# Kernel tuning notes

Hardware: AMD Instinct MI355X
Metric: run time of the kernel (lower is better)

## Reference

```python
import jax, jax.numpy as jnp
import numpy as np

N_ATOMS = 32768
N_GRAPHS = 256
PER_GRAPH = 128
HIDDEN = 128
FILTERS = 128
NUM_GAUSS = 50
CUTOFF = 5.0
NUM_LAYERS = 3
OUT_CH = 1
BOX = 14.1
SLOPE = 0.015


def _lrelu(x):
    return jnp.where(x > 0, x, SLOPE * x)


def setup_inputs() -> dict:
    rng = np.random.default_rng(0)
    batch = np.repeat(np.arange(N_GRAPHS), PER_GRAPH).astype(np.int64)
    pos_np = rng.uniform(0.0, BOX, size=(N_ATOMS, 3)).astype(np.float32)
    # radius graph, built per-graph exactly like compute_radius_graph
    # (with global index offset so edges reference global node ids)
    edges = []
    for b in range(N_GRAPHS):
        pb = pos_np[b * PER_GRAPH:(b + 1) * PER_GRAPH]
        d = np.linalg.norm(pb[:, None, :] - pb[None, :, :], axis=-1)
        src, dst = np.where((d <= CUTOFF) & (d > 0))
        edges.append(np.stack([src, dst], axis=0) + b * PER_GRAPH)
    edge_index = np.concatenate(edges, axis=1).astype(np.int64)
    z = rng.integers(0, 100, size=(N_ATOMS,)).astype(np.int64)

    key = jax.random.key(0)
    ks = jax.random.split(key, 12)

    def xavier(k, shape):
        fan_in, fan_out = shape[-2], shape[-1]
        s = float(np.sqrt(6.0 / (fan_in + fan_out)))
        return jax.random.uniform(k, shape, jnp.float32, -s, s)

    L = NUM_LAYERS
    params = dict(
        emb=jax.random.normal(ks[0], (100, HIDDEN), jnp.float32),
        w_lin=xavier(ks[1], (L, HIDDEN, FILTERS)),
        mlp_w1=xavier(ks[2], (L, NUM_GAUSS, FILTERS)), mlp_b1=jnp.zeros((L, FILTERS), jnp.float32),
        mlp_w2=xavier(ks[3], (L, FILTERS, FILTERS)), mlp_b2=jnp.zeros((L, FILTERS), jnp.float32),
        mlp_w3=xavier(ks[4], (L, FILTERS, FILTERS)), mlp_b3=jnp.zeros((L, FILTERS), jnp.float32),
        lout_w=xavier(ks[5], (L, FILTERS, FILTERS)), lout_b=jnp.zeros((L, FILTERS), jnp.float32),
        v_w1=xavier(ks[6], (L, FILTERS, HIDDEN)), v_b1=jnp.zeros((L, HIDDEN), jnp.float32),
        v_w2=xavier(ks[7], (L, HIDDEN, HIDDEN)), v_b2=jnp.zeros((L, HIDDEN), jnp.float32),
        u_w1=xavier(ks[8], (HIDDEN, HIDDEN // 2)), u_b1=jnp.zeros((HIDDEN // 2,), jnp.float32),
        u_w2=xavier(ks[9], (HIDDEN // 2, OUT_CH)), u_b2=jnp.zeros((OUT_CH,), jnp.float32),
    )
    return dict(z=jnp.asarray(z), pos=jnp.asarray(pos_np), batch=jnp.asarray(batch),
                edge_index=jnp.asarray(edge_index), **params)


def reference(z, pos, batch, edge_index, emb, w_lin,
              mlp_w1, mlp_b1, mlp_w2, mlp_b2, mlp_w3, mlp_b3,
              lout_w, lout_b, v_w1, v_b1, v_w2, v_b2,
              u_w1, u_b1, u_w2, u_b2):
    row, col = edge_index[0], edge_index[1]          # row = j (source), col = i (target)
    dist = jnp.linalg.norm(pos[row] - pos[col], axis=-1)        # [E]
    offset = jnp.linspace(0.0, CUTOFF, NUM_GAUSS)
    coeff = -0.5 / (offset[1] - offset[0]) ** 2
    dist_emb = jnp.exp(coeff * (dist[:, None] - offset[None, :]) ** 2)   # [E, G]
    C = 0.5 * (jnp.cos(dist * jnp.pi / CUTOFF) + 1.0)                    # [E]

    v = emb[z]                                                           # [N, H]
    for l in range(NUM_LAYERS):
        # UpdateE: filter MLP on distance embedding, cosine cutoff envelope
        h = _lrelu(dist_emb @ mlp_w1[l] + mlp_b1[l])
        h = _lrelu(h @ mlp_w2[l] + mlp_b2[l])
        W = (h @ mlp_w3[l] + mlp_b3[l]) * C[:, None]                     # [E, F]
        e = (v @ w_lin[l])[row] * W                                      # gather + modulate
        e = (e @ lout_w[l] + lout_b[l]) + e                              # residual edge lin
        # UpdateV: scatter-add into target nodes, then 2-layer MLP residual
        agg = jax.ops.segment_sum(e, col, num_segments=N_ATOMS)         # [N, F]
        v = v + (_lrelu(agg @ v_w1[l] + v_b1[l]) @ v_w2[l] + v_b2[l])

    # UpdateU: node MLP then per-graph mean pooling
    u = _lrelu(v @ u_w1 + u_b1) @ u_w2 + u_b2                            # [N, out]
    sums = jax.ops.segment_sum(u, batch, num_segments=N_GRAPHS)
    cnt = jax.ops.segment_sum(jnp.ones((u.shape[0],), u.dtype), batch, num_segments=N_GRAPHS)
    return jnp.where(cnt[:, None] > 0, sums / jnp.maximum(cnt, 1.0)[:, None], 0.0)
```

## Files before the change

### kernel.cpp

```cpp
#include <hip/hip_runtime.h>

typedef float f4 __attribute__((ext_vector_type(4)));
typedef float f2 __attribute__((ext_vector_type(2)));
typedef float f32x4 __attribute__((ext_vector_type(4)));
typedef short bf16x8 __attribute__((ext_vector_type(8)));
typedef short sh4 __attribute__((ext_vector_type(4)));
typedef unsigned short us4 __attribute__((ext_vector_type(4)));

#define G_TAB 8192
#define SWZ(row, b) ((b) ^ (((row) & 7) << 4))

__device__ __forceinline__ float lrelu(float x) { return x > 0.f ? x : 0.015f * x; }

__device__ __forceinline__ short f2bf(float x) {
  union { float f; unsigned u; } v; v.f = x;
  unsigned r = v.u + 0x7fff + ((v.u >> 16) & 1);
  return (short)(r >> 16);
}
__device__ __forceinline__ float bf2f(short h) {
  union { float f; unsigned u; } v; v.u = ((unsigned)(unsigned short)h) << 16;
  return v.f;
}
__device__ __forceinline__ float bf2fu(unsigned short h) {
  union { float f; unsigned u; } v; v.u = ((unsigned)h) << 16;
  return v.f;
}

__device__ __forceinline__ void st_pair(short* Hi, short* Lo, int row, int k, f4 x) {
  sh4 hi, lo;
  #pragma unroll
  for (int c = 0; c < 4; c++) { hi[c] = f2bf(x[c]); lo[c] = f2bf(x[c] - bf2f(hi[c])); }
  int b = row * 256 + SWZ(row, (k >> 3) * 16) + (k & 7) * 2;
  *(sh4*)((char*)Hi + b) = hi;
  *(sh4*)((char*)Lo + b) = lo;
}
__device__ __forceinline__ void st_pair1(short* Hi, short* Lo, int row, int k, float x) {
  short hi = f2bf(x), lo = f2bf(x - bf2f(hi));
  int b = row * 256 + SWZ(row, (k >> 3) * 16) + (k & 7) * 2;
  *(short*)((char*)Hi + b) = hi;
  *(short*)((char*)Lo + b) = lo;
}

template<int NFC, int CH>
__device__ __forceinline__ void mm16(const short* Ahi, const short* Alo,
    const short* __restrict__ BhT, const short* __restrict__ BlT,
    int w, int l, f32x4* acc) {
  int lr = l & 15, lk = l >> 4;
  #pragma unroll
  for (int fc = 0; fc < NFC; fc++) acc[fc] = (f32x4)0.f;
  #pragma unroll
  for (int ch = 0; ch < CH; ch++) {
    int arow = w * 16 + lr;
    int ab = arow * 256 + SWZ(arow, ch * 64 + lk * 16);
    bf16x8 ah = *(const bf16x8*)((const char*)Ahi + ab);
    bf16x8 al = *(const bf16x8*)((const char*)Alo + ab);
    #pragma unroll
    for (int fc = 0; fc < NFC; fc++) {
      int bcol = fc * 16 + lr;
      int bb = bcol * 256 + SWZ(bcol, ch * 64 + lk * 16);
      bf16x8 bh = *(const bf16x8*)((const char*)BhT + bb);
      bf16x8 bl = *(const bf16x8*)((const char*)BlT + bb);
      acc[fc] = __builtin_amdgcn_mfma_f32_16x16x32_bf16(ah, bh, acc[fc], 0, 0, 0);
      acc[fc] = __builtin_amdgcn_mfma_f32_16x16x32_bf16(al, bh, acc[fc], 0, 0, 0);
      acc[fc] = __builtin_amdgcn_mfma_f32_16x16x32_bf16(ah, bl, acc[fc], 0, 0, 0);
    }
  }
}


__global__ __launch_bounds__(256) void gather_emb(const int* __restrict__ z,
    const float* __restrict__ emb, float* __restrict__ v, int nf4) {
  int i = blockIdx.x * 256 + threadIdx.x;
  if (i >= nf4) return;
  int a = i >> 5, s = i & 31;
  ((f4*)v)[i] = ((const f4*)emb)[z[a] * 32 + s];
}

__global__ __launch_bounds__(256) void edge_geom(const int* __restrict__ ei,
    const float* __restrict__ pos, float* __restrict__ edc, int E) {
  int e = blockIdx.x * 256 + threadIdx.x;
  if (e >= E) return;
  int r = ei[e], c = ei[E + e];
  float dx = pos[3*r] - pos[3*c];
  float dy = pos[3*r+1] - pos[3*c+1];
  float dz = pos[3*r+2] - pos[3*c+2];
  float d = sqrtf(dx*dx + dy*dy + dz*dz);
  edc[2*e] = d;
  edc[2*e+1] = 0.5f * (cosf(d * 0.6283185307179586f) + 1.0f);
}

__global__ __launch_bounds__(256) void make_starts(const int* __restrict__ row,
    int* __restrict__ starts, int E, int N) {
  int i = blockIdx.x * 256 + threadIdx.x;
  if (i > N) return;
  int lo = 0, hi = E;
  while (lo < hi) { int mid = (lo + hi) >> 1; if (row[mid] < i) lo = mid + 1; else hi = mid; }
  starts[i] = lo;
}

__global__ __launch_bounds__(256) void convert_wt(const float* __restrict__ w_lin,
    const float* __restrict__ vw2, const float* __restrict__ uw1,
    const float* __restrict__ mw1, const float* __restrict__ mw2,
    const float* __restrict__ mw3, const float* __restrict__ vw1,
    short* __restrict__ dhi, short* __restrict__ dlo) {
  int y = blockIdx.y;
  int i = blockIdx.x * 256 + threadIdx.x;
  int k = i >> 7, j = i & 127;
  int slot; float x;
  if (y < 3)       { slot = y;     x = w_lin[(size_t)y*16384 + k*128 + j]; }
  else if (y < 6)  { slot = 3 + y; x = vw2[(size_t)(y-3)*16384 + k*128 + j]; }
  else if (y == 6) { slot = 9;     x = (j < 64) ? uw1[k*64 + j] : 0.f; }
  else if (y < 10) { slot = 3 + y; x = mw2[(size_t)(y-7)*16384 + k*128 + j]; }
  else if (y < 13) { slot = 3 + y; x = mw3[(size_t)(y-10)*16384 + k*128 + j]; }
  else if (y < 16) { slot = 3 + y; x = (k < 50) ? mw1[(size_t)(y-13)*6400 + k*128 + j] : 0.f; }
  else             { slot = 3 + y; x = vw1[(size_t)(y-16)*16384 + k*128 + j]; }
  short hi = f2bf(x);
  int ob = j * 256 + (((k >> 3) * 16) ^ ((j & 7) << 4)) + (k & 7) * 2;
  char* bh = (char*)dhi + (size_t)slot * 32768;
  char* bl = (char*)dlo + (size_t)slot * 32768;
  *(short*)(bh + ob) = hi;
  *(short*)(bl + ob) = f2bf(x - bf2f(hi));
}

__global__ __launch_bounds__(128) void make_c1(const float* __restrict__ lball,
    const float* __restrict__ w1all, float* __restrict__ c1all) {
  int l = blockIdx.y;
  const float* lb = lball + (size_t)l * 128;
  const float* w1 = w1all + (size_t)l * 16384;
  int j = threadIdx.x;
  float s = 0.f;
  for (int k = 0; k < 128; k++) s += lb[k] * w1[k * 128 + j];
  c1all[l * 128 + j] = s;
}

__global__ __launch_bounds__(512) void prep_M(const float* __restrict__ loutw,
    short* __restrict__ whiT, short* __restrict__ wloT) {
  __shared__ __align__(16) short Ahi[16384];
  __shared__ __align__(16) short Alo[16384];
  int tid = threadIdx.x;
  int lay = blockIdx.x;
  int w = tid >> 6, l = tid & 63;
  int lr = l & 15, lk = l >> 4;
  int arow = w * 16 + (l >> 2), sub = l & 3;
  const f4* src = (const f4*)(loutw + (size_t)lay*16384 + (size_t)arow*128 + sub*32);
  #pragma unroll
  for (int q = 0; q < 8; q++) {
    f4 x = src[q];
    int kb = sub * 32 + q * 4;
    #pragma unroll
    for (int cc = 0; cc < 4; cc++) if (arow == kb + cc) x[cc] += 1.0f;
    st_pair(Ahi, Alo, arow, kb, x);
  }
  __syncthreads();
  f32x4 acc[8];
  mm16<8,4>(Ahi, Alo, whiT + (size_t)(19+lay)*16384, wloT + (size_t)(19+lay)*16384, w, l, acc);
  char* bh = (char*)whiT + (size_t)(3+lay) * 32768;
  char* bl = (char*)wloT + (size_t)(3+lay) * 32768;
  #pragma unroll
  for (int r = 0; r < 4; r++)
    #pragma unroll
    for (int fc = 0; fc < 8; fc++) {
      int row = w*16 + lk*4 + r, col = fc*16 + lr;
      float val = acc[fc][r];
      short hi = f2bf(val);
      int ob = col * 256 + (((row >> 3) * 16) ^ ((col & 7) << 4)) + (row & 7) * 2;
      *(short*)(bh + ob) = hi;
      *(short*)(bl + ob) = f2bf(val - bf2f(hi));
    }
}

__global__ __launch_bounds__(512) void table_mfma(
    const short* __restrict__ whiT, const short* __restrict__ wloT,
    const float* __restrict__ mb1, const float* __restrict__ mb2,
    const float* __restrict__ mb3, unsigned short* __restrict__ tables) {
  __shared__ __align__(16) short Ahi[16384];
  __shared__ __align__(16) short Alo[16384];
  __shared__ __align__(16) short Bhi[16384];
  __shared__ __align__(16) short Blo[16384];
  int tid = threadIdx.x;
  int lay = blockIdx.y;
  int p0 = blockIdx.x * 128;
  int w = tid >> 6, l = tid & 63;
  int lr = l & 15, lk = l >> 4;
  int prow = w * 16 + (l >> 2), sub = l & 3;
  const float delta = 5.0f / (G_TAB - 1);
  {
    float d = (p0 + prow) * delta;
    #pragma unroll
    for (int q = 0; q < 4; q++) {
      f4 x;
      #pragma unroll
      for (int cc = 0; cc < 4; cc++) {
        int k = sub * 16 + q * 4 + cc;
        float t = d - k * (5.0f / 49.0f);
        x[cc] = (k < 50) ? expf(-48.02f * t * t) : 0.f;
      }
      st_pair(Ahi, Alo, prow, sub * 16 + q * 4, x);
    }
  }
  __syncthreads();
  f32x4 acc[8];
  mm16<8,2>(Ahi, Alo, whiT + (size_t)(16+lay)*16384, wloT + (size_t)(16+lay)*16384, w, l, acc);
  #pragma unroll
  for (int r = 0; r < 4; r++)
    #pragma unroll
    for (int fc = 0; fc < 8; fc++)
      st_pair1(Bhi, Blo, w*16 + lk*4 + r, fc*16 + lr,
               lrelu(acc[fc][r] + mb1[lay*128 + fc*16 + lr]));
  __syncthreads();
  mm16<8,4>(Bhi, Blo, whiT + (size_t)(10+lay)*16384, wloT + (size_t)(10+lay)*16384, w, l, acc);
  #pragma unroll
  for (int r = 0; r < 4; r++)
    #pragma unroll
    for (int fc = 0; fc < 8; fc++)
      st_pair1(Ahi, Alo, w*16 + lk*4 + r, fc*16 + lr,
               lrelu(acc[fc][r] + mb2[lay*128 + fc*16 + lr]));
  __syncthreads();
  mm16<8,4>(Ahi, Alo, whiT + (size_t)(13+lay)*16384, wloT + (size_t)(13+lay)*16384, w, l, acc);
  unsigned short* tb = tables + (size_t)lay * G_TAB * 128;
  #pragma unroll
  for (int r = 0; r < 4; r++)
    #pragma unroll
    for (int fc = 0; fc < 8; fc++)
      tb[(size_t)(p0 + w*16 + lk*4 + r) * 128 + fc*16 + lr] =
          (unsigned short)f2bf(acc[fc][r] + mb3[lay*128 + fc*16 + lr]);
}


template<int ACT, int ACC, int BIAS>
__global__ __launch_bounds__(256) void gemm128b(
    const float* __restrict__ A, const short* __restrict__ BhS,
    const short* __restrict__ BlS, const float* __restrict__ bias,
    const float* __restrict__ bias2, const float* __restrict__ rs,
    float* __restrict__ out) {
  __shared__ __align__(16) short Bhi[16384];
  int tid = threadIdx.x;
  int p = blockIdx.x;
  size_t row0 = (size_t)(((p & 7) << 5) + (p >> 3)) * 128;
  #pragma unroll
  for (int s = 0; s < 8; s++)
    ((bf16x8*)Bhi)[tid + 256*s] = ((const bf16x8*)BhS)[tid + 256*s];
  __syncthreads();
  int w = tid >> 6, l = tid & 63, lr = l & 15, lk = l >> 4;
  const char* BlB = (const char*)BlS;
  #pragma unroll
  for (int half = 0; half < 2; half++) {
    int rbase = half * 64 + w * 16;
    const float* ap0 = A + (row0 + rbase + lr) * 128;
    bf16x8 ah[4], al[4];
    #pragma unroll
    for (int ch = 0; ch < 4; ch++) {
      const f4* ap = (const f4*)(ap0 + ch*32 + lk*8);
      f4 x0 = ap[0], x1 = ap[1];
      #pragma unroll
      for (int c = 0; c < 4; c++) {
        short h0 = f2bf(x0[c]);
        ah[ch][c] = h0; al[ch][c] = f2bf(x0[c] - bf2f(h0));
        short h1 = f2bf(x1[c]);
        ah[ch][c+4] = h1; al[ch][c+4] = f2bf(x1[c] - bf2f(h1));
      }
    }
    f32x4 acc[8];
    #pragma unroll
    for (int fc = 0; fc < 8; fc++) acc[fc] = (f32x4)0.f;
    #pragma unroll
    for (int ch = 0; ch < 4; ch++)
      #pragma unroll
      for (int fc = 0; fc < 8; fc++) {
        int bcol = fc*16 + lr;
        int bb = bcol*256 + SWZ(bcol, ch*64 + lk*16);
        bf16x8 bh = *(const bf16x8*)((const char*)Bhi + bb);
        bf16x8 bl = *(const bf16x8*)(BlB + bb);
        acc[fc] = __builtin_amdgcn_mfma_f32_16x16x32_bf16(ah[ch], bh, acc[fc], 0, 0, 0);
        acc[fc] = __builtin_amdgcn_mfma_f32_16x16x32_bf16(al[ch], bh, acc[fc], 0, 0, 0);
        acc[fc] = __builtin_amdgcn_mfma_f32_16x16x32_bf16(ah[ch], bl, acc[fc], 0, 0, 0);
      }
    #pragma unroll
    for (int r = 0; r < 4; r++) {
      size_t grow = row0 + rbase + lk*4 + r;
      float rsv = (BIAS == 3) ? rs[grow] : 0.f;
      #pragma unroll
      for (int fc = 0; fc < 8; fc++) {
        int col = fc*16 + lr;
        float val = acc[fc][r];
        if (BIAS == 1) val += bias[col];
        if (BIAS == 3) val += rsv * bias[col] + bias2[col];
        if (ACT) val = lrelu(val);
        float* op = &out[grow * 128 + col];
        if (ACC) val += *op;
        *op = val;
      }
    }
  }
}

__global__ __launch_bounds__(256) void edge_gather(
    const int* __restrict__ ei, const int* __restrict__ starts,
    const float* __restrict__ edc, const float* __restrict__ vlin,
    const unsigned short* __restrict__ tb, float* __restrict__ S,
    float* __restrict__ deg, int E, int N) {
  int tid = threadIdx.x;
  int lane = tid & 63, grp = tid >> 6;
  int half = lane >> 5, fl = lane & 31;
  int p = blockIdx.x;
  int o = ((p & 7) << 10) + (p >> 3);
  int a = o * 4 + grp;
  if (a >= N) return;
  int s = starts[a], ee = starts[a + 1];
  int mid = s + ((ee - s + 1) >> 1);
  int e0 = half ? mid : s;
  int e1 = half ? ee : mid;
  int j0 = fl * 4;
  const float sc = (float)(G_TAB - 1) / 5.0f;
  f4 acc = (f4)0.f;
  int e = e0;
  for (; e + 3 < e1; e += 4) {
    int cc[4]; f2 dd[4];
    #pragma unroll
    for (int q = 0; q < 4; q++) { cc[q] = ei[E + e + q]; dd[q] = *(const f2*)&edc[2*(e+q)]; }
    f4 vl[4]; us4 t[4];
    #pragma unroll
    for (int q = 0; q < 4; q++) {
      int i0 = (int)(dd[q][0] * sc + 0.5f);
      if (i0 > G_TAB - 1) i0 = G_TAB - 1;
      t[q] = *(const us4*)&tb[(size_t)i0 * 128 + j0];
      vl[q] = *(const f4*)&vlin[(size_t)cc[q] * 128 + j0];
    }
    #pragma unroll
    for (int q = 0; q < 4; q++) {
      f4 T;
      #pragma unroll
      for (int c4 = 0; c4 < 4; c4++) T[c4] = bf2fu(t[q][c4]);
      acc += vl[q] * (T * dd[q][1]);
    }
  }
  for (; e < e1; e++) {
    int c0 = ei[E + e];
    f2 dc0 = *(const f2*)&edc[2 * e];
    int i0 = (int)(dc0[0] * sc + 0.5f);
    if (i0 > G_TAB - 1) i0 = G_TAB - 1;
    us4 t = *(const us4*)&tb[(size_t)i0 * 128 + j0];
    f4 vl = *(const f4*)&vlin[(size_t)c0 * 128 + j0];
    f4 T;
    #pragma unroll
    for (int c4 = 0; c4 < 4; c4++) T[c4] = bf2fu(t[c4]);
    acc += vl * (T * dc0[1]);
  }
  #pragma unroll
  for (int c4 = 0; c4 < 4; c4++) acc[c4] += __shfl_xor(acc[c4], 32);
  if (half == 0) *(f4*)&S[(size_t)a * 128 + j0] = acc;
  if (lane == 0) deg[a] = (float)(ee - s);
}

__global__ __launch_bounds__(256) void readout_b(const float* __restrict__ v,
    const short* __restrict__ Bh9, const short* __restrict__ Bl9,
    const float* __restrict__ ub1, const float* __restrict__ uw2,
    float* __restrict__ y) {
  __shared__ __align__(16) short Bh[8192];
  int tid = threadIdx.x;
  int p = blockIdx.x;
  size_t row0 = (size_t)(((p & 7) << 5) + (p >> 3)) * 128;
  #pragma unroll
  for (int s = 0; s < 4; s++)
    ((bf16x8*)Bh)[tid + 256*s] = ((const bf16x8*)Bh9)[tid + 256*s];
  __syncthreads();
  int w = tid >> 6, l = tid & 63, lr = l & 15, lk = l >> 4;
  const char* BlB = (const char*)Bl9;
  #pragma unroll
  for (int half = 0; half < 2; half++) {
    int rbase = half * 64 + w * 16;
    const float* ap0 = v + (row0 + rbase + lr) * 128;
    bf16x8 ah[4], al[4];
    #pragma unroll
    for (int ch = 0; ch < 4; ch++) {
      const f4* ap = (const f4*)(ap0 + ch*32 + lk*8);
      f4 x0 = ap[0], x1 = ap[1];
      #pragma unroll
      for (int c = 0; c < 4; c++) {
        short h0 = f2bf(x0[c]);
        ah[ch][c] = h0; al[ch][c] = f2bf(x0[c] - bf2f(h0));
        short h1 = f2bf(x1[c]);
        ah[ch][c+4] = h1; al[ch][c+4] = f2bf(x1[c] - bf2f(h1));
      }
    }
    f32x4 acc[4];
    #pragma unroll
    for (int fc = 0; fc < 4; fc++) acc[fc] = (f32x4)0.f;
    #pragma unroll
    for (int ch = 0; ch < 4; ch++)
      #pragma unroll
      for (int fc = 0; fc < 4; fc++) {
        int bcol = fc*16 + lr;
        int bb = bcol*256 + SWZ(bcol, ch*64 + lk*16);
        bf16x8 bh = *(const bf16x8*)((const char*)Bh + bb);
        bf16x8 bl = *(const bf16x8*)(BlB + bb);
        acc[fc] = __builtin_amdgcn_mfma_f32_16x16x32_bf16(ah[ch], bh, acc[fc], 0, 0, 0);
        acc[fc] = __builtin_amdgcn_mfma_f32_16x16x32_bf16(al[ch], bh, acc[fc], 0, 0, 0);
        acc[fc] = __builtin_amdgcn_mfma_f32_16x16x32_bf16(ah[ch], bl, acc[fc], 0, 0, 0);
      }
    #pragma unroll
    for (int r = 0; r < 4; r++) {
      float sv = 0.f;
      #pragma unroll
      for (int fc = 0; fc < 4; fc++) {
        int col = fc*16 + lr;
        sv += lrelu(acc[fc][r] + ub1[col]) * uw2[col];
      }
      sv += __shfl_xor(sv, 1); sv += __shfl_xor(sv, 2);
      sv += __shfl_xor(sv, 4); sv += __shfl_xor(sv, 8);
      if (lr == 0) y[row0 + rbase + lk*4 + r] = sv;
    }
  }
}

__global__ __launch_bounds__(256) void graph_mean(const float* __restrict__ y,
    const float* __restrict__ ub2, float* __restrict__ out) {
  __shared__ float red[256];
  int tid = threadIdx.x;
  red[tid] = y[blockIdx.x * 256 + tid];
  __syncthreads();
  for (int s = 64; s > 0; s >>= 1) {
    if ((tid & 127) < s) red[tid] += red[tid + s];
    __syncthreads();
  }
  if ((tid & 127) == 0)
    out[blockIdx.x * 2 + (tid >> 7)] = red[tid] * (1.0f / 128.0f) + ub2[0];
}

extern "C" void kernel_launch(void* const* d_in, const int* in_sizes, int n_in,
                              void* d_out, int out_size, void* d_ws, size_t ws_size,
                              hipStream_t stream) {
  const int*   z     = (const int*)d_in[0];
  const float* pos   = (const float*)d_in[1];
  const int*   ei    = (const int*)d_in[3];
  const float* emb   = (const float*)d_in[4];
  const float* w_lin = (const float*)d_in[5];
  const float* mw1   = (const float*)d_in[6];
  const float* mb1   = (const float*)d_in[7];
  const float* mw2   = (const float*)d_in[8];
  const float* mb2   = (const float*)d_in[9];
  const float* mw3   = (const float*)d_in[10];
  const float* mb3   = (const float*)d_in[11];
  const float* loutw = (const float*)d_in[12];
  const float* loutb = (const float*)d_in[13];
  const float* vw1   = (const float*)d_in[14];
  const float* vb1   = (const float*)d_in[15];
  const float* vw2   = (const float*)d_in[16];
  const float* vb2   = (const float*)d_in[17];
  const float* uw1   = (const float*)d_in[18];
  const float* ub1   = (const float*)d_in[19];
  const float* uw2   = (const float*)d_in[20];
  const float* ub2   = (const float*)d_in[21];
  int N = in_sizes[0];
  int E = in_sizes[3] / 2;
  float* out = (float*)d_out;

  size_t off = 0;
  auto alloc = [&](size_t bytes) -> void* {
    void* p = (char*)d_ws + off;
    off += (bytes + 255) & ~(size_t)255;
    return p;
  };
  float* v      = (float*)alloc((size_t)N * 128 * 4);
  float* bufA   = (float*)alloc((size_t)N * 128 * 4);
  float* bufB   = (float*)alloc((size_t)N * 128 * 4);
  float* bufC   = (float*)alloc((size_t)N * 128 * 4);
  unsigned short* tables = (unsigned short*)alloc((size_t)3 * G_TAB * 128 * 2);
  short* whiT   = (short*)alloc((size_t)22 * 16384 * 2);
  short* wloT   = (short*)alloc((size_t)22 * 16384 * 2);
  float* c1s    = (float*)alloc(3 * 128 * 4);
  float* deg    = (float*)alloc((size_t)N * 4);
  float* edc    = (float*)alloc((size_t)E * 8);
  int*   starts = (int*)alloc((size_t)(N + 1) * 4);
  float* y      = (float*)alloc((size_t)N * 4);

  gather_emb<<<(N * 32 + 255) / 256, 256, 0, stream>>>(z, emb, v, N * 32);
  edge_geom<<<(E + 255) / 256, 256, 0, stream>>>(ei, pos, edc, E);
  make_starts<<<(N + 256) / 256, 256, 0, stream>>>(ei, starts, E, N);
  convert_wt<<<dim3(64, 19), 256, 0, stream>>>(w_lin, vw2, uw1, mw1, mw2, mw3, vw1,
                                               whiT, wloT);
  prep_M<<<3, 512, 0, stream>>>(loutw, whiT, wloT);
  make_c1<<<dim3(1, 3), 128, 0, stream>>>(loutb, vw1, c1s);
  table_mfma<<<dim3(G_TAB / 128, 3), 512, 0, stream>>>(whiT, wloT, mb1, mb2, mb3, tables);

  for (int l = 0; l < 3; l++) {
    gemm128b<0, 0, 0><<<N / 128, 256, 0, stream>>>(
        v, whiT + (size_t)l * 16384, wloT + (size_t)l * 16384,
        nullptr, nullptr, nullptr, bufA);
    edge_gather<<<N / 4, 256, 0, stream>>>(ei, starts, edc, bufA,
                                           tables + (size_t)l * G_TAB * 128,
                                           bufB, deg, E, N);
    gemm128b<1, 0, 3><<<N / 128, 256, 0, stream>>>(
        bufB, whiT + (size_t)(3 + l) * 16384, wloT + (size_t)(3 + l) * 16384,
        c1s + (size_t)l * 128, vb1 + (size_t)l * 128, deg, bufC);
    gemm128b<0, 1, 1><<<N / 128, 256, 0, stream>>>(
        bufC, whiT + (size_t)(6 + l) * 16384, wloT + (size_t)(6 + l) * 16384,
        vb2 + (size_t)l * 128, nullptr, nullptr, v);
  }
  readout_b<<<N / 128, 256, 0, stream>>>(v, whiT + (size_t)9 * 16384,
                                         wloT + (size_t)9 * 16384, ub1, uw2, y);
  graph_mean<<<N / 256, 256, 0, stream>>>(y, ub2, out);
}
```

Baseline: 268.5 us.

## Store intermediate activations in bf16 and drop the low-part MFMA for bf16 inputs

```diff
diff --git a/kernel.cpp b/kernel.cpp
--- a/kernel.cpp
+++ b/kernel.cpp
@@ -1,4 +1,5 @@
 #include <hip/hip_runtime.h>
+#include <hip/hip_bf16.h>
 
 typedef float f4 __attribute__((ext_vector_type(4)));
 typedef float f2 __attribute__((ext_vector_type(2)));
@@ -13,13 +14,12 @@
 __device__ __forceinline__ float lrelu(float x) { return x > 0.f ? x : 0.015f * x; }
 
 __device__ __forceinline__ short f2bf(float x) {
-  union { float f; unsigned u; } v; v.f = x;
-  unsigned r = v.u + 0x7fff + ((v.u >> 16) & 1);
-  return (short)(r >> 16);
+  __hip_bfloat16 h = __float2bfloat16(x);
+  return *reinterpret_cast<short*>(&h);
 }
 __device__ __forceinline__ float bf2f(short h) {
-  union { float f; unsigned u; } v; v.u = ((unsigned)(unsigned short)h) << 16;
-  return v.f;
+  __hip_bfloat16 b = *reinterpret_cast<__hip_bfloat16*>(&h);
+  return __bfloat162float(b);
 }
 __device__ __forceinline__ float bf2fu(unsigned short h) {
   union { float f; unsigned u; } v; v.u = ((unsigned)h) << 16;
@@ -227,12 +227,12 @@
 }
 
 
-template<int ACT, int ACC, int BIAS>
+template<int ACT, int ACC, int BIAS, int ABF, int OBF>
 __global__ __launch_bounds__(256) void gemm128b(
-    const float* __restrict__ A, const short* __restrict__ BhS,
+    const void* __restrict__ Ain, const short* __restrict__ BhS,
     const short* __restrict__ BlS, const float* __restrict__ bias,
     const float* __restrict__ bias2, const float* __restrict__ rs,
-    float* __restrict__ out) {
+    void* __restrict__ outv) {
   __shared__ __align__(16) short Bhi[16384];
   int tid = threadIdx.x;
   int p = blockIdx.x;
@@ -246,18 +246,25 @@
   #pragma unroll
   for (int half = 0; half < 2; half++) {
     int rbase = half * 64 + w * 16;
-    const float* ap0 = A + (row0 + rbase + lr) * 128;
     bf16x8 ah[4], al[4];
-    #pragma unroll
-    for (int ch = 0; ch < 4; ch++) {
-      const f4* ap = (const f4*)(ap0 + ch*32 + lk*8);
-      f4 x0 = ap[0], x1 = ap[1];
-      #pragma unroll
-      for (int c = 0; c < 4; c++) {
-        short h0 = f2bf(x0[c]);
-        ah[ch][c] = h0; al[ch][c] = f2bf(x0[c] - bf2f(h0));
-        short h1 = f2bf(x1[c]);
-        ah[ch][c+4] = h1; al[ch][c+4] = f2bf(x1[c] - bf2f(h1));
+    if (ABF) {
+      const short* ap0 = (const short*)Ain + (row0 + rbase + lr) * 128;
+      #pragma unroll
+      for (int ch = 0; ch < 4; ch++)
+        ah[ch] = *(const bf16x8*)(ap0 + ch*32 + lk*8);
+    } else {
+      const float* ap0 = (const float*)Ain + (row0 + rbase + lr) * 128;
+      #pragma unroll
+      for (int ch = 0; ch < 4; ch++) {
+        const f4* ap = (const f4*)(ap0 + ch*32 + lk*8);
+        f4 x0 = ap[0], x1 = ap[1];
+        #pragma unroll
+        for (int c = 0; c < 4; c++) {
+          short h0 = f2bf(x0[c]);
+          ah[ch][c] = h0; al[ch][c] = f2bf(x0[c] - bf2f(h0));
+          short h1 = f2bf(x1[c]);
+          ah[ch][c+4] = h1; al[ch][c+4] = f2bf(x1[c] - bf2f(h1));
+        }
       }
     }
     f32x4 acc[8];
@@ -272,7 +279,8 @@
         bf16x8 bh = *(const bf16x8*)((const char*)Bhi + bb);
         bf16x8 bl = *(const bf16x8*)(BlB + bb);
         acc[fc] = __builtin_amdgcn_mfma_f32_16x16x32_bf16(ah[ch], bh, acc[fc], 0, 0, 0);
-        acc[fc] = __builtin_amdgcn_mfma_f32_16x16x32_bf16(al[ch], bh, acc[fc], 0, 0, 0);
+        if (!ABF)
+          acc[fc] = __builtin_amdgcn_mfma_f32_16x16x32_bf16(al[ch], bh, acc[fc], 0, 0, 0);
         acc[fc] = __builtin_amdgcn_mfma_f32_16x16x32_bf16(ah[ch], bl, acc[fc], 0, 0, 0);
       }
     #pragma unroll
@@ -286,9 +294,13 @@
         if (BIAS == 1) val += bias[col];
         if (BIAS == 3) val += rsv * bias[col] + bias2[col];
         if (ACT) val = lrelu(val);
-        float* op = &out[grow * 128 + col];
-        if (ACC) val += *op;
-        *op = val;
+        if (OBF) {
+          ((short*)outv)[grow * 128 + col] = f2bf(val);
+        } else {
+          float* op = (float*)outv + grow * 128 + col;
+          if (ACC) val += *op;
+          *op = val;
+        }
       }
     }
   }
@@ -296,7 +308,7 @@
 
 __global__ __launch_bounds__(256) void edge_gather(
     const int* __restrict__ ei, const int* __restrict__ starts,
-    const float* __restrict__ edc, const float* __restrict__ vlin,
+    const float* __restrict__ edc, const unsigned short* __restrict__ vlinb,
     const unsigned short* __restrict__ tb, float* __restrict__ S,
     float* __restrict__ deg, int E, int N) {
   int tid = threadIdx.x;
@@ -318,20 +330,20 @@
     int cc[4]; f2 dd[4];
     #pragma unroll
     for (int q = 0; q < 4; q++) { cc[q] = ei[E + e + q]; dd[q] = *(const f2*)&edc[2*(e+q)]; }
-    f4 vl[4]; us4 t[4];
+    us4 vl[4], t[4];
     #pragma unroll
     for (int q = 0; q < 4; q++) {
       int i0 = (int)(dd[q][0] * sc + 0.5f);
       if (i0 > G_TAB - 1) i0 = G_TAB - 1;
       t[q] = *(const us4*)&tb[(size_t)i0 * 128 + j0];
-      vl[q] = *(const f4*)&vlin[(size_t)cc[q] * 128 + j0];
+      vl[q] = *(const us4*)&vlinb[(size_t)cc[q] * 128 + j0];
     }
     #pragma unroll
     for (int q = 0; q < 4; q++) {
-      f4 T;
-      #pragma unroll
-      for (int c4 = 0; c4 < 4; c4++) T[c4] = bf2fu(t[q][c4]);
-      acc += vl[q] * (T * dd[q][1]);
+      f4 T, V;
+      #pragma unroll
+      for (int c4 = 0; c4 < 4; c4++) { T[c4] = bf2fu(t[q][c4]); V[c4] = bf2fu(vl[q][c4]); }
+      acc += V * (T * dd[q][1]);
     }
   }
   for (; e < e1; e++) {
@@ -340,11 +352,11 @@
     int i0 = (int)(dc0[0] * sc + 0.5f);
     if (i0 > G_TAB - 1) i0 = G_TAB - 1;
     us4 t = *(const us4*)&tb[(size_t)i0 * 128 + j0];
-    f4 vl = *(const f4*)&vlin[(size_t)c0 * 128 + j0];
-    f4 T;
-    #pragma unroll
-    for (int c4 = 0; c4 < 4; c4++) T[c4] = bf2fu(t[c4]);
-    acc += vl * (T * dc0[1]);
+    us4 vl = *(const us4*)&vlinb[(size_t)c0 * 128 + j0];
+    f4 T, V;
+    #pragma unroll
+    for (int c4 = 0; c4 < 4; c4++) { T[c4] = bf2fu(t[c4]); V[c4] = bf2fu(vl[c4]); }
+    acc += V * (T * dc0[1]);
   }
   #pragma unroll
   for (int c4 = 0; c4 < 4; c4++) acc[c4] += __shfl_xor(acc[c4], 32);
@@ -462,9 +474,9 @@
     return p;
   };
   float* v      = (float*)alloc((size_t)N * 128 * 4);
-  float* bufA   = (float*)alloc((size_t)N * 128 * 4);
-  float* bufB   = (float*)alloc((size_t)N * 128 * 4);
-  float* bufC   = (float*)alloc((size_t)N * 128 * 4);
+  unsigned short* vlinb = (unsigned short*)alloc((size_t)N * 128 * 2);
+  float* Sbuf   = (float*)alloc((size_t)N * 128 * 4);
+  short* t16    = (short*)alloc((size_t)N * 128 * 2);
   unsigned short* tables = (unsigned short*)alloc((size_t)3 * G_TAB * 128 * 2);
   short* whiT   = (short*)alloc((size_t)22 * 16384 * 2);
   short* wloT   = (short*)alloc((size_t)22 * 16384 * 2);
@@ -484,17 +496,17 @@
   table_mfma<<<dim3(G_TAB / 128, 3), 512, 0, stream>>>(whiT, wloT, mb1, mb2, mb3, tables);
 
   for (int l = 0; l < 3; l++) {
-    gemm128b<0, 0, 0><<<N / 128, 256, 0, stream>>>(
+    gemm128b<0, 0, 0, 0, 1><<<N / 128, 256, 0, stream>>>(
         v, whiT + (size_t)l * 16384, wloT + (size_t)l * 16384,
-        nullptr, nullptr, nullptr, bufA);
-    edge_gather<<<N / 4, 256, 0, stream>>>(ei, starts, edc, bufA,
+        nullptr, nullptr, nullptr, vlinb);
+    edge_gather<<<N / 4, 256, 0, stream>>>(ei, starts, edc, vlinb,
                                            tables + (size_t)l * G_TAB * 128,
-                                           bufB, deg, E, N);
-    gemm128b<1, 0, 3><<<N / 128, 256, 0, stream>>>(
-        bufB, whiT + (size_t)(3 + l) * 16384, wloT + (size_t)(3 + l) * 16384,
-        c1s + (size_t)l * 128, vb1 + (size_t)l * 128, deg, bufC);
-    gemm128b<0, 1, 1><<<N / 128, 256, 0, stream>>>(
-        bufC, whiT + (size_t)(6 + l) * 16384, wloT + (size_t)(6 + l) * 16384,
+                                           Sbuf, deg, E, N);
+    gemm128b<1, 0, 3, 0, 1><<<N / 128, 256, 0, stream>>>(
+        Sbuf, whiT + (size_t)(3 + l) * 16384, wloT + (size_t)(3 + l) * 16384,
+        c1s + (size_t)l * 128, vb1 + (size_t)l * 128, deg, t16);
+    gemm128b<0, 1, 1, 1, 0><<<N / 128, 256, 0, stream>>>(
+        t16, whiT + (size_t)(6 + l) * 16384, wloT + (size_t)(6 + l) * 16384,
         vb2 + (size_t)l * 128, nullptr, nullptr, v);
   }
   readout_b<<<N / 128, 256, 0, stream>>>(v, whiT + (size_t)9 * 16384,
```

Result: slower. 345.3 us (+28.6%).
